# Kernel optimization log

Hardware: AMD Instinct MI355X
Metric: run time of the kernel (lower is better)

## Reference

```python
import jax, jax.numpy as jnp
import numpy as np

B, C_IN, C_OUT, H, F_DIM = 32, 64, 1, 4096, 8
OUT_CH, K = F_DIM + 1, F_DIM // 2 + 1          # even-feature branch: 9 channels, kernel (1,5)
HALF = F_DIM * (F_DIM + 1) // 2                # 36 upper-triangular entries
MIN_VEC = 0.001
IU = np.triu_indices(F_DIM)                    # torch.triu_indices(f, f)


def setup_inputs() -> dict:
    key = jax.random.key(0)
    k1, k2, k3, k4, k5 = jax.random.split(key, 5)
    x = jax.random.normal(k1, (B, C_IN, H, F_DIM), jnp.float32)
    w_n = jax.random.normal(k2, (C_OUT, C_IN, 1, 1), jnp.float32) * 0.05
    b_n = jax.random.normal(k3, (C_OUT,), jnp.float32) * 0.05
    w_p = jax.random.normal(k4, (OUT_CH, C_IN, 1, K), jnp.float32) * 0.05
    b_p = jax.random.normal(k5, (OUT_CH,), jnp.float32) * 0.05
    return {"x": x, "w_n": w_n, "b_n": b_n, "w_p": w_p, "b_p": b_p}


def _forward(x, w_n, b_n, w_p, b_p):
    # n_conv: 1x1 conv -> softplus  (loc: [B, C_OUT, H, F_DIM])
    loc = jax.nn.softplus(
        jnp.einsum('bchw,oc->bohw', x, w_n[:, :, 0, 0]) + b_n[None, :, None, None])
    # p_conv: (1,K) valid conv -> softplus  (scale: [B, OUT_CH, H, W_out])
    p = jax.lax.conv_general_dilated(
        x, w_p, window_strides=(1, 1), padding='VALID',
        dimension_numbers=('NCHW', 'OIHW', 'NCHW')) + b_p[None, :, None, None]
    scale = jax.nn.softplus(p)
    # unsqueeze(1) + permute(0,1,3,2,4) + flatten(start_dim=3) -> [B,1,H,HALF]
    sigma = jnp.transpose(scale, (0, 2, 1, 3)).reshape(B, 1, H, HALF)
    # scatter upper-tri values symmetrically into [B,1,H,F,F]
    z = jnp.zeros((B, 1, H, F_DIM, F_DIM), sigma.dtype)
    z = z.at[..., IU[0], IU[1]].set(sigma)
    z = z.at[..., IU[1], IU[0]].set(sigma)
    # batched eigh, clamp eigenvalues, reconstruct PD matrix, symmetrize
    eigval, eigvec = jnp.linalg.eigh(z)
    clamped = jnp.maximum(eigval, MIN_VEC)
    pd = jnp.einsum('...ij,...j,...kj->...ik', eigvec, clamped, eigvec)
    pd = 0.5 * (pd + jnp.swapaxes(pd, -1, -2))
    return loc, pd


def reference(x, w_n, b_n, w_p, b_p):
    return _forward(x, w_n, b_n, w_p, b_p)
```

## Files before the change

### kernel.cpp

```cpp
#include <hip/hip_runtime.h>
#include <math.h>

#define B_      32
#define C_IN    64
#define H_      4096
#define F_      8
#define OUT_CH  9
#define KW      5
#define BH      (B_ * H_)
#define LOC_N   (BH * F_)
#define NSWEEP  6
#define MIN_VEC 0.001f
#define LSTR    65

__device__ const int PAIRS[7][4][2] = {
  {{0,7},{1,6},{2,5},{3,4}},
  {{0,6},{5,7},{1,4},{2,3}},
  {{0,5},{4,6},{3,7},{1,2}},
  {{0,4},{3,5},{2,6},{1,7}},
  {{0,3},{2,4},{1,5},{6,7}},
  {{0,2},{1,3},{4,7},{5,6}},
  {{0,1},{2,7},{3,6},{4,5}},
};

#define SYM(i,j) (((i) < (j)) ? A[i][j] : A[j][i])

__device__ __forceinline__ float softplus_f(float v) {
    return fmaxf(v, 0.0f) + __logf(1.0f + __expf(-fabsf(v)));
}

__global__ __launch_bounds__(256, 2)
void mgauss_fused(const float* __restrict__ x,
                  const float* __restrict__ w_n,
                  const float* __restrict__ b_n,
                  const float* __restrict__ w_p,
                  const float* __restrict__ b_p,
                  float* __restrict__ out)
{
    __shared__ float xsh[128][LSTR];

    const int tid  = threadIdx.x;
    const int wv   = tid >> 6;
    const int lane = tid & 63;
    const int halfsel = wv >> 1;
    const int pl   = ((wv & 1) << 6) | lane;
    const int t    = blockIdx.x * 128 + pl;
    const int b    = t >> 12;
    const int h    = t & 4095;

    const float* xp = x + ((size_t)b * C_IN * H_ + h) * F_;
    const int c0 = __builtin_amdgcn_readfirstlane(halfsel << 5);

    float acc[44];
    #pragma unroll
    for (int k = 0; k < 44; ++k) acc[k] = 0.0f;

    #pragma unroll 4
    for (int c = 0; c < 32; ++c) {
        const int cc = c0 + c;
        const float4 x0 = *(const float4*)(xp + (size_t)cc * (H_ * F_));
        const float4 x1 = *(const float4*)(xp + (size_t)cc * (H_ * F_) + 4);
        const float xa[F_] = {x0.x, x0.y, x0.z, x0.w, x1.x, x1.y, x1.z, x1.w};

        const float wn = w_n[cc];
        #pragma unroll
        for (int w = 0; w < F_; ++w) acc[w] = fmaf(xa[w], wn, acc[w]);

        #pragma unroll
        for (int o = 0; o < OUT_CH; ++o) {
            #pragma unroll
            for (int k = 0; k < KW; ++k) {
                const float wvp = w_p[(o * C_IN + cc) * KW + k];
                #pragma unroll
                for (int wo = 0; wo < 4; ++wo)
                    acc[8 + o * 4 + wo] = fmaf(xa[wo + k], wvp, acc[8 + o * 4 + wo]);
            }
        }
    }

    if (halfsel) {
        #pragma unroll
        for (int k = 0; k < 44; ++k) xsh[pl][k] = acc[k];
    }
    __syncthreads();
    if (!halfsel) {
        #pragma unroll
        for (int k = 0; k < 44; ++k) acc[k] += xsh[pl][k];
        #pragma unroll
        for (int k = 8; k < 44; ++k) xsh[pl][k] = acc[k];
    }
    __syncthreads();
    if (halfsel) {
        #pragma unroll
        for (int k = 8; k < 44; ++k) acc[k] = xsh[pl][k];
    }

    if (!halfsel) {
        const float bn = b_n[0];
        float lv[F_];
        #pragma unroll
        for (int w = 0; w < F_; ++w) lv[w] = softplus_f(acc[w] + bn);
        float* lo = out + (size_t)t * F_;
        *(float4*)(lo)     = make_float4(lv[0], lv[1], lv[2], lv[3]);
        *(float4*)(lo + 4) = make_float4(lv[4], lv[5], lv[6], lv[7]);
    }

    float A[F_][F_];
    {
        float sig[36];
        #pragma unroll
        for (int o = 0; o < OUT_CH; ++o) {
            const float bp = b_p[o];
            #pragma unroll
            for (int wo = 0; wo < 4; ++wo)
                sig[o * 4 + wo] = softplus_f(acc[8 + o * 4 + wo] + bp);
        }
        int k = 0;
        #pragma unroll
        for (int i = 0; i < F_; ++i)
            #pragma unroll
            for (int j = i; j < F_; ++j) {
                A[i][j] = sig[k];
                ++k;
            }
    }

    const int myBase = halfsel << 2;
    float Vh[4][F_];
    #pragma unroll
    for (int i = 0; i < 4; ++i)
        #pragma unroll
        for (int j = 0; j < F_; ++j)
            Vh[i][j] = (myBase + i == j) ? 1.0f : 0.0f;

    for (int sweep = 0; sweep < NSWEEP; ++sweep) {
        #pragma unroll
        for (int r = 0; r < 7; ++r) {
            float cs[4], sn[4], tv[4];
            #pragma unroll
            for (int j = 0; j < 4; ++j) {
                const int p = PAIRS[r][j][0], q = PAIRS[r][j][1];
                const float apq = A[p][q];
                const float app = A[p][p];
                const float aqq = A[q][q];
                const float th = (aqq - app) * 0.5f * __builtin_amdgcn_rcpf(apq);
                float tt = __builtin_amdgcn_rcpf(fabsf(th) +
                              __builtin_amdgcn_sqrtf(fmaf(th, th, 1.0f)));
                tt = (th < 0.0f) ? -tt : tt;
                tt = (apq == 0.0f) ? 0.0f : tt;
                const float cc = __builtin_amdgcn_rsqf(fmaf(tt, tt, 1.0f));
                cs[j] = cc; sn[j] = tt * cc; tv[j] = tt;
            }
            #pragma unroll
            for (int j = 0; j < 4; ++j) {
                const int p = PAIRS[r][j][0], q = PAIRS[r][j][1];
                const float cc = cs[j], ss = sn[j], tt = tv[j];
                const float apq = A[p][q];
                A[p][p] = fmaf(-tt, apq, A[p][p]);
                A[q][q] = fmaf( tt, apq, A[q][q]);
                A[p][q] = 0.0f;
                #pragma unroll
                for (int i = 0; i < F_; ++i) {
                    if (i == p || i == q) continue;
                    const float aip = SYM(i, p);
                    const float aiq = SYM(i, q);
                    SYM(i, p) = fmaf(-ss, aiq, cc * aip);
                    SYM(i, q) = fmaf( ss, aip, cc * aiq);
                }
            }
            #pragma unroll
            for (int j = 0; j < 4; ++j) {
                const int p = PAIRS[r][j][0], q = PAIRS[r][j][1];
                const float cc = cs[j], ss = sn[j];
                #pragma unroll
                for (int i = 0; i < 4; ++i) {
                    const float u = Vh[i][p], v = Vh[i][q];
                    Vh[i][p] = fmaf(-ss, v, cc * u);
                    Vh[i][q] = fmaf( ss, u, cc * v);
                }
            }
        }
    }

    float lam[F_];
    #pragma unroll
    for (int k = 0; k < F_; ++k) lam[k] = fmaxf(A[k][k], MIN_VEC);

    __syncthreads();
    {
        const int moff = myBase << 3;
        #pragma unroll
        for (int i = 0; i < 4; ++i)
            #pragma unroll
            for (int j = 0; j < F_; ++j)
                xsh[pl][moff + (i << 3) + j] = Vh[i][j];
    }
    __syncthreads();
    float Vo[4][F_];
    {
        const int ooff = (myBase ^ 4) << 3;
        #pragma unroll
        for (int i = 0; i < 4; ++i)
            #pragma unroll
            for (int j = 0; j < F_; ++j)
                Vo[i][j] = xsh[pl][ooff + (i << 3) + j];
    }

    float W[4][F_];
    #pragma unroll
    for (int i = 0; i < 4; ++i)
        #pragma unroll
        for (int k = 0; k < F_; ++k)
            W[i][k] = Vh[i][k] * lam[k];

    float* po = out + LOC_N + (size_t)t * (F_ * F_) + myBase * F_;
    #pragma unroll
    for (int r = 0; r < 4; ++r) {
        float pa[4], pb[4];
        #pragma unroll
        for (int s = 0; s < 4; ++s) {
            float a0 = 0.0f, b0 = 0.0f;
            #pragma unroll
            for (int k = 0; k < F_; ++k) {
                a0 = fmaf(W[r][k], Vh[s][k], a0);
                b0 = fmaf(W[r][k], Vo[s][k], b0);
            }
            pa[s] = a0; pb[s] = b0;
        }
        float* pr = po + r * F_;
        *(float4*)(pr + myBase)       = make_float4(pa[0], pa[1], pa[2], pa[3]);
        *(float4*)(pr + (myBase ^ 4)) = make_float4(pb[0], pb[1], pb[2], pb[3]);
    }
}

extern "C" void kernel_launch(void* const* d_in, const int* in_sizes, int n_in,
                              void* d_out, int out_size, void* d_ws, size_t ws_size,
                              hipStream_t stream) {
    const float* x   = (const float*)d_in[0];
    const float* w_n = (const float*)d_in[1];
    const float* b_n = (const float*)d_in[2];
    const float* w_p = (const float*)d_in[3];
    const float* b_p = (const float*)d_in[4];
    float* out = (float*)d_out;

    dim3 grid(BH / 128);
    dim3 block(256);
    hipLaunchKernelGGL(mgauss_fused, grid, block, 0, stream,
                       x, w_n, b_n, w_p, b_p, out);
}
```

Baseline: 460.9 us.

## Cut Jacobi sweeps, prefetch x loads, and share softplus results via LDS

Reduces the Jacobi eigen-solver from six to five sweeps, cutting rotation arithmetic per matrix. Restructures the channel reduction loop with explicit register double-buffering of x loads to overlap memory latency with FMAs. Computes the scale softplus once in one half-block and shares the 36 sigma values through LDS instead of recomputing them in both halves. Fewer sweeps risks slightly less converged eigenvalues for ill-conditioned matrices.

After: 463.9 us. About the same (+0.7%).

```diff
diff --git a/kernel.cpp b/kernel.cpp
--- a/kernel.cpp
+++ b/kernel.cpp
@@ -9,7 +9,7 @@
 #define KW      5
 #define BH      (B_ * H_)
 #define LOC_N   (BH * F_)
-#define NSWEEP  6
+#define NSWEEP  5
 #define MIN_VEC 0.001f
 #define LSTR    65
 
@@ -55,47 +55,75 @@
     #pragma unroll
     for (int k = 0; k < 44; ++k) acc[k] = 0.0f;
 
-    #pragma unroll 4
-    for (int c = 0; c < 32; ++c) {
-        const int cc = c0 + c;
-        const float4 x0 = *(const float4*)(xp + (size_t)cc * (H_ * F_));
-        const float4 x1 = *(const float4*)(xp + (size_t)cc * (H_ * F_) + 4);
-        const float xa[F_] = {x0.x, x0.y, x0.z, x0.w, x1.x, x1.y, x1.z, x1.w};
-
-        const float wn = w_n[cc];
-        #pragma unroll
-        for (int w = 0; w < F_; ++w) acc[w] = fmaf(xa[w], wn, acc[w]);
-
+    {
+        const size_t CSTR = (size_t)H_ * F_;
+        const float* xq = xp + (size_t)c0 * CSTR;
+        float4 pf0[2], pf1[2];
+        #pragma unroll
+        for (int j = 0; j < 2; ++j) {
+            pf0[j] = *(const float4*)(xq + (size_t)j * CSTR);
+            pf1[j] = *(const float4*)(xq + (size_t)j * CSTR + 4);
+        }
+        #pragma unroll
+        for (int g = 0; g < 16; ++g) {
+            float4 cur0[2], cur1[2];
+            #pragma unroll
+            for (int j = 0; j < 2; ++j) { cur0[j] = pf0[j]; cur1[j] = pf1[j]; }
+            if (g < 15) {
+                #pragma unroll
+                for (int j = 0; j < 2; ++j) {
+                    pf0[j] = *(const float4*)(xq + (size_t)((g + 1) * 2 + j) * CSTR);
+                    pf1[j] = *(const float4*)(xq + (size_t)((g + 1) * 2 + j) * CSTR + 4);
+                }
+            }
+            #pragma unroll
+            for (int j = 0; j < 2; ++j) {
+                const int cc = c0 + g * 2 + j;
+                const float xa[F_] = {cur0[j].x, cur0[j].y, cur0[j].z, cur0[j].w,
+                                      cur1[j].x, cur1[j].y, cur1[j].z, cur1[j].w};
+
+                const float wn = w_n[cc];
+                #pragma unroll
+                for (int w = 0; w < F_; ++w) acc[w] = fmaf(xa[w], wn, acc[w]);
+
+                #pragma unroll
+                for (int o = 0; o < OUT_CH; ++o) {
+                    #pragma unroll
+                    for (int k = 0; k < KW; ++k) {
+                        const float wvp = w_p[(o * C_IN + cc) * KW + k];
+                        #pragma unroll
+                        for (int wo = 0; wo < 4; ++wo)
+                            acc[8 + o * 4 + wo] = fmaf(xa[wo + k], wvp, acc[8 + o * 4 + wo]);
+                    }
+                }
+            }
+        }
+    }
+
+    if (halfsel) {
+        #pragma unroll
+        for (int k = 0; k < 44; ++k) xsh[pl][k] = acc[k];
+    }
+    __syncthreads();
+    float sig[36];
+    if (!halfsel) {
+        #pragma unroll
+        for (int k = 0; k < 44; ++k) acc[k] += xsh[pl][k];
         #pragma unroll
         for (int o = 0; o < OUT_CH; ++o) {
-            #pragma unroll
-            for (int k = 0; k < KW; ++k) {
-                const float wvp = w_p[(o * C_IN + cc) * KW + k];
-                #pragma unroll
-                for (int wo = 0; wo < 4; ++wo)
-                    acc[8 + o * 4 + wo] = fmaf(xa[wo + k], wvp, acc[8 + o * 4 + wo]);
-            }
-        }
-    }
-
+            const float bp = b_p[o];
+            #pragma unroll
+            for (int wo = 0; wo < 4; ++wo)
+                sig[o * 4 + wo] = softplus_f(acc[8 + o * 4 + wo] + bp);
+        }
+        #pragma unroll
+        for (int k = 0; k < 36; ++k) xsh[pl][k] = sig[k];
+    }
+    __syncthreads();
     if (halfsel) {
         #pragma unroll
-        for (int k = 0; k < 44; ++k) xsh[pl][k] = acc[k];
-    }
-    __syncthreads();
-    if (!halfsel) {
-        #pragma unroll
-        for (int k = 0; k < 44; ++k) acc[k] += xsh[pl][k];
-        #pragma unroll
-        for (int k = 8; k < 44; ++k) xsh[pl][k] = acc[k];
-    }
-    __syncthreads();
-    if (halfsel) {
-        #pragma unroll
-        for (int k = 8; k < 44; ++k) acc[k] = xsh[pl][k];
-    }
-
-    if (!halfsel) {
+        for (int k = 0; k < 36; ++k) sig[k] = xsh[pl][k];
+    } else {
         const float bn = b_n[0];
         float lv[F_];
         #pragma unroll
@@ -107,14 +135,6 @@
 
     float A[F_][F_];
     {
-        float sig[36];
-        #pragma unroll
-        for (int o = 0; o < OUT_CH; ++o) {
-            const float bp = b_p[o];
-            #pragma unroll
-            for (int wo = 0; wo < 4; ++wo)
-                sig[o * 4 + wo] = softplus_f(acc[8 + o * 4 + wo] + bp);
-        }
         int k = 0;
         #pragma unroll
         for (int i = 0; i < F_; ++i)
```
